# Kernel tuning notes

Measured on AMD Instinct MI355X. Metric: run time of the kernel, lower is better.

## Reference

```python
import jax, jax.numpy as jnp
import numpy as np

B, L, D, H = 4, 2048, 512, 512


def setup_inputs() -> dict:
    key = jax.random.key(0)
    ks = jax.random.split(key, 7)
    scale = D ** (-0.5)
    return {
        "x": jax.random.normal(ks[0], (B, L, D), jnp.float32),
        "hidden": jax.random.normal(ks[1], (B, D, H), jnp.float32),
        "log_base_lr": jnp.asarray(np.log(0.01), jnp.float32),
        "log_base_weight_decay": jnp.asarray(np.log(0.99), jnp.float32),
        "Wq": jax.random.normal(ks[2], (H, D), jnp.float32) * scale,
        "Wk": jax.random.normal(ks[3], (H, D), jnp.float32) * scale,
        "Wv": jax.random.normal(ks[4], (D, D), jnp.float32) * scale,
        "fc_lr_w": jax.random.normal(ks[5], (1, D), jnp.float32) * scale,
        "fc_lr_b": jnp.zeros((1,), jnp.float32),
        "fc_wd_w": jax.random.normal(ks[6], (1, D), jnp.float32) * scale,
        "fc_wd_b": jnp.zeros((1,), jnp.float32),
    }


def reference(x, hidden, log_base_lr, log_base_weight_decay, Wq, Wk, Wv,
              fc_lr_w, fc_lr_b, fc_wd_w, fc_wd_b):
    b, l, d = x.shape
    W_prev = hidden                                      # (b, d, h)
    query = jnp.einsum('bld,hd->blh', x, Wq)             # (b, l, h)
    key = jnp.einsum('bld,hd->blh', x, Wk)               # (b, l, h)
    value = jnp.einsum('bld,ed->ble', x, Wv)             # (b, l, d)

    lr = jnp.exp(log_base_lr) * jax.nn.sigmoid(
        jnp.einsum('bld,d->bl', x, fc_lr_w[0]) + fc_lr_b[0])        # (b, l)
    log_weight_decay = jnp.log(
        jnp.exp(log_base_weight_decay) * jax.nn.sigmoid(
            jnp.einsum('bld,d->bl', x, fc_wd_w[0]) + fc_wd_b[0]))   # (b, l)

    # cross-chunk decay: exp of prefix-sum of log decays
    wd_cross = jnp.exp(jnp.cumsum(log_weight_decay, axis=1))        # (b, l)

    # inner-chunk decay mask: (b, m, l), strictly-upper cumsum then upper triu
    rep = jnp.broadcast_to(log_weight_decay[:, None, :], (b, l, l))
    wd_inner = jnp.triu(jnp.exp(jnp.cumsum(jnp.triu(rep, 1), axis=2)))

    kq = jnp.einsum('blh,bmh->blm', key, query)          # (b, l, m)
    mask_kq = kq * wd_inner                              # (b, l, m)

    WpK_V = jnp.einsum('bdh,blh->bld', W_prev, key) - value         # (b, l, d)

    y_inner = -jnp.einsum('bld,bl,blm->bld', WpK_V, lr, mask_kq)
    y_cross = jnp.einsum('bdh,blh,bl->bld', W_prev, key, wd_cross)
    y = y_inner + y_cross

    W_next_inner = -jnp.einsum('bld,bl,blh->bdh', WpK_V, lr * wd_inner[:, :, -1], key)
    W_next_cross = W_prev * wd_cross[:, -1][:, None, None]
    W_next = W_next_inner + W_next_cross
    return (y, W_next)
```

## Files before the change

### kernel.cpp

```cpp
#include <hip/hip_runtime.h>
#include <cstdint>
#include <cstddef>

#define B_ 4
#define L_ 2048
#define D_ 512
#define H_ 512
#define CH 64
#define NC (L_ / CH)
#define NS 4

typedef unsigned short u16;
typedef __attribute__((ext_vector_type(8))) short short8v;
typedef __attribute__((ext_vector_type(4))) float f32x4;

typedef __attribute__((address_space(3))) unsigned lds_uint;
typedef const __attribute__((address_space(1))) unsigned glob_uint;

__device__ __forceinline__ void glds16(const u16* g, const u16* l) {
    __builtin_amdgcn_global_load_lds((glob_uint*)g, (lds_uint*)l, 16, 0, 0);
}

__device__ __forceinline__ u16 bf16_rne(float x) {
    union { float f; unsigned u; } v; v.f = x;
    unsigned r = v.u + 0x7fffu + ((v.u >> 16) & 1u);
    return (u16)(r >> 16);
}
__device__ __forceinline__ float bf16_tof(u16 h) {
    union { unsigned u; float f; } v; v.u = ((unsigned)h) << 16;
    return v.f;
}

__global__ __launch_bounds__(256) void k_prep(
    const float* __restrict__ x, const float* __restrict__ flr_w, const float* __restrict__ flr_b,
    const float* __restrict__ fwd_w, const float* __restrict__ fwd_b,
    const float* __restrict__ lblr, const float* __restrict__ lbwd,
    float* __restrict__ lr, float* __restrict__ lwd, float* __restrict__ wd,
    u16* __restrict__ xh)
{
    int bx = blockIdx.x;
    int wave = threadIdx.x >> 6;
    int lane = threadIdx.x & 63;
    int row  = bx * 4 + wave;
    const float4* xr = (const float4*)(x + (size_t)row * D_);
    const float4* wl = (const float4*)flr_w;
    const float4* ww = (const float4*)fwd_w;
    float zl = 0.f, zw = 0.f;
#pragma unroll
    for (int i = 0; i < 2; ++i) {
        int idx = lane + i * 64;
        float4 xv = xr[idx];
        float4 av = wl[idx];
        float4 bv = ww[idx];
        zl += xv.x*av.x + xv.y*av.y + xv.z*av.z + xv.w*av.w;
        zw += xv.x*bv.x + xv.y*bv.y + xv.z*bv.z + xv.w*bv.w;
        ushort4 h4;
        h4.x = bf16_rne(xv.x); h4.y = bf16_rne(xv.y);
        h4.z = bf16_rne(xv.z); h4.w = bf16_rne(xv.w);
        *(ushort4*)(xh + (size_t)row * D_ + idx * 4) = h4;
    }
#pragma unroll
    for (int off = 32; off; off >>= 1) {
        zl += __shfl_xor(zl, off, 64);
        zw += __shfl_xor(zw, off, 64);
    }
    if (lane == 0) {
        zl += flr_b[0];
        zw += fwd_b[0];
        float lrv = expf(lblr[0]) / (1.f + expf(-zl));
        float ls = (zw >= 0.f) ? (-log1pf(expf(-zw))) : (zw - log1pf(expf(zw)));
        float lw = lbwd[0] + ls;
        lr[row]  = lrv;
        lwd[row] = lw;
        wd[row]  = expf(lw);
    }
}

__global__ __launch_bounds__(256) void k_cumsum(
    const float* __restrict__ lwd, const float* __restrict__ lr,
    const float* __restrict__ Wq, const float* __restrict__ Wk, const float* __restrict__ Wv,
    const float* __restrict__ hid,
    u16* __restrict__ Wqh, u16* __restrict__ Wkh, u16* __restrict__ Wvh, u16* __restrict__ Wph,
    float* __restrict__ cum, float* __restrict__ wdc, float* __restrict__ c)
{
    int bx = blockIdx.x;
    if (bx >= B_) {
        int idx = bx - B_;
        int y = idx >> 8;
        const size_t DH = (size_t)D_ * H_;
        const float* s; u16* d;
        if      (y == 0) { s = Wq; d = Wqh; }
        else if (y == 1) { s = Wk; d = Wkh; }
        else if (y == 2) { s = Wv; d = Wvh; }
        else             { s = hid + (size_t)(y - 3) * DH; d = Wph + (size_t)(y - 3) * DH; }
        int i = ((idx & 255) * 256 + threadIdx.x) * 4;
        float4 v = *(const float4*)(s + i);
        ushort4 h4;
        h4.x = bf16_rne(v.x); h4.y = bf16_rne(v.y);
        h4.z = bf16_rne(v.z); h4.w = bf16_rne(v.w);
        *(ushort4*)(d + i) = h4;
        return;
    }
    int b = bx;
    int t = threadIdx.x;
    const float* in = lwd + (size_t)b * L_;
    float v[8];
    float s = 0.f;
#pragma unroll
    for (int j = 0; j < 8; ++j) { s += in[t*8 + j]; v[j] = s; }
    __shared__ float sd[256];
    __shared__ float totb;
    sd[t] = s;
    __syncthreads();
    for (int d = 1; d < 256; d <<= 1) {
        float xv = (t >= d) ? sd[t - d] : 0.f;
        __syncthreads();
        sd[t] += xv;
        __syncthreads();
    }
    float excl = sd[t] - s;
    if (t == 255) totb = sd[255];
    __syncthreads();
    float total = totb;
#pragma unroll
    for (int j = 0; j < 8; ++j) {
        int l = t*8 + j;
        float cv = excl + v[j];
        cum[(size_t)b*L_ + l] = cv;
        wdc[(size_t)b*L_ + l] = expf(cv);
        c[(size_t)b*L_ + l]   = lr[(size_t)b*L_ + l] * expf(total - cv);
    }
}


#define MFMA8(accv, A0v, A1v, B0v, B1v, B2v, B3v) \
    accv[0][0] = __builtin_amdgcn_mfma_f32_16x16x32_bf16(A0v, B0v, accv[0][0], 0, 0, 0); \
    accv[0][1] = __builtin_amdgcn_mfma_f32_16x16x32_bf16(A0v, B1v, accv[0][1], 0, 0, 0); \
    accv[0][2] = __builtin_amdgcn_mfma_f32_16x16x32_bf16(A0v, B2v, accv[0][2], 0, 0, 0); \
    accv[0][3] = __builtin_amdgcn_mfma_f32_16x16x32_bf16(A0v, B3v, accv[0][3], 0, 0, 0); \
    accv[1][0] = __builtin_amdgcn_mfma_f32_16x16x32_bf16(A1v, B0v, accv[1][0], 0, 0, 0); \
    accv[1][1] = __builtin_amdgcn_mfma_f32_16x16x32_bf16(A1v, B1v, accv[1][1], 0, 0, 0); \
    accv[1][2] = __builtin_amdgcn_mfma_f32_16x16x32_bf16(A1v, B2v, accv[1][2], 0, 0, 0); \
    accv[1][3] = __builtin_amdgcn_mfma_f32_16x16x32_bf16(A1v, B3v, accv[1][3], 0, 0, 0);

struct GemmGeom {
    size_t gA, gB0, gB1;
    int dA, dB0, dB1;
    int offA[2], offB[4];
};
__device__ __forceinline__ void gg_init(GemmGeom& G, int lda, int ldb, int m0, int n0) {
    const int tid  = threadIdx.x;
    const int lane = tid & 63;
    const int wv = tid >> 6, wm = wv >> 1, wn_ = wv & 1;
    const int rA = tid >> 2;
    G.gA = (size_t)(m0 + rA) * lda + (((tid & 3) ^ ((rA >> 1) & 3)) * 8);
    G.dA = wv * 1024;
    {
        int r = tid >> 2, s = tid & 3;
        G.gB0 = (size_t)(n0 + r) * ldb + ((s ^ ((r >> 1) & 3)) * 8);
        G.dB0 = wv * 1024;
        int flat = 256 + tid;
        r = flat >> 2; s = flat & 3;
        G.gB1 = (size_t)(n0 + r) * ldb + ((s ^ ((r >> 1) & 3)) * 8);
        G.dB1 = 4096 + wv * 1024;
    }
#pragma unroll
    for (int mf = 0; mf < 2; ++mf) {
        int ra = wm * 32 + mf * 16 + (lane & 15);
        G.offA[mf] = ra * 64 + (((lane >> 4) ^ ((ra >> 1) & 3)) * 16);
    }
#pragma unroll
    for (int nf = 0; nf < 4; ++nf) {
        int rb = wn_ * 64 + nf * 16 + (lane & 15);
        G.offB[nf] = rb * 64 + (((lane >> 4) ^ ((rb >> 1) & 3)) * 16);
    }
}

__device__ __forceinline__ void mfma_nt_dualB(
    char* smem, const u16* __restrict__ A_g,
    const u16* __restrict__ B0_g, const u16* __restrict__ B1_g,
    int lda, int ldb, int K, int m0, int n0, f32x4 acc0[2][4], f32x4 acc1[2][4])
{
    GemmGeom G; gg_init(G, lda, ldb, m0, n0);
    auto stage = [&](int bi, int k0) {
        glds16(A_g  + G.gA  + k0, (const u16*)(smem + bi * 4096 + G.dA));
        glds16(B0_g + G.gB0 + k0, (const u16*)(smem + 8192  + bi * 8192 + G.dB0));
        glds16(B0_g + G.gB1 + k0, (const u16*)(smem + 8192  + bi * 8192 + G.dB1));
        glds16(B1_g + G.gB0 + k0, (const u16*)(smem + 24576 + bi * 8192 + G.dB0));
        glds16(B1_g + G.gB1 + k0, (const u16*)(smem + 24576 + bi * 8192 + G.dB1));
    };
    const int nt = K >> 5;
    stage(0, 0);
    if (nt > 1) stage(1, 32);
    for (int t = 0; t < nt; ++t) {
        const int bi = t & 1;
        if (t + 1 < nt) asm volatile("s_waitcnt vmcnt(5)" ::: "memory");
        else            asm volatile("s_waitcnt vmcnt(0)" ::: "memory");
        __builtin_amdgcn_s_barrier();
        asm volatile("" ::: "memory");
        const char* bA  = smem + bi * 4096;
        const char* bB0 = smem + 8192  + bi * 8192;
        const char* bB1 = smem + 24576 + bi * 8192;
        short8v a0 = *(const short8v*)(bA + G.offA[0]);
        short8v a1 = *(const short8v*)(bA + G.offA[1]);
        short8v p0 = *(const short8v*)(bB0 + G.offB[0]);
        short8v p1 = *(const short8v*)(bB0 + G.offB[1]);
        short8v p2 = *(const short8v*)(bB0 + G.offB[2]);
        short8v p3 = *(const short8v*)(bB0 + G.offB[3]);
        short8v q0 = *(const short8v*)(bB1 + G.offB[0]);
        short8v q1 = *(const short8v*)(bB1 + G.offB[1]);
        short8v q2 = *(const short8v*)(bB1 + G.offB[2]);
        short8v q3 = *(const short8v*)(bB1 + G.offB[3]);
        __builtin_amdgcn_s_setprio(1);
        MFMA8(acc0, a0, a1, p0, p1, p2, p3)
        MFMA8(acc1, a0, a1, q0, q1, q2, q3)
        __builtin_amdgcn_s_setprio(0);
        asm volatile("" ::: "memory");
        __builtin_amdgcn_s_barrier();
        asm volatile("" ::: "memory");
        if (t + 2 < nt) stage(bi, (t + 2) << 5);
    }
}

__device__ __forceinline__ void mfma_nt_dualAB(
    char* smem, const u16* __restrict__ A0_g, const u16* __restrict__ A1_g,
    const u16* __restrict__ B0_g, const u16* __restrict__ B1_g,
    int lda, int ldb, int K, int m0, int n0, f32x4 acc0[2][4], f32x4 acc1[2][4])
{
    GemmGeom G; gg_init(G, lda, ldb, m0, n0);
    auto stage = [&](int bi, int k0) {
        glds16(A0_g + G.gA  + k0, (const u16*)(smem + bi * 4096 + G.dA));
        glds16(A1_g + G.gA  + k0, (const u16*)(smem + 8192 + bi * 4096 + G.dA));
        glds16(B0_g + G.gB0 + k0, (const u16*)(smem + 16384 + bi * 8192 + G.dB0));
        glds16(B0_g + G.gB1 + k0, (const u16*)(smem + 16384 + bi * 8192 + G.dB1));
        glds16(B1_g + G.gB0 + k0, (const u16*)(smem + 32768 + bi * 8192 + G.dB0));
        glds16(B1_g + G.gB1 + k0, (const u16*)(smem + 32768 + bi * 8192 + G.dB1));
    };
    const int nt = K >> 5;
    stage(0, 0);
    if (nt > 1) stage(1, 32);
    for (int t = 0; t < nt; ++t) {
        const int bi = t & 1;
        if (t + 1 < nt) asm volatile("s_waitcnt vmcnt(6)" ::: "memory");
        else            asm volatile("s_waitcnt vmcnt(0)" ::: "memory");
        __builtin_amdgcn_s_barrier();
        asm volatile("" ::: "memory");
        const char* bA0 = smem + bi * 4096;
        const char* bA1 = smem + 8192  + bi * 4096;
        const char* bB0 = smem + 16384 + bi * 8192;
        const char* bB1 = smem + 32768 + bi * 8192;
        short8v a0 = *(const short8v*)(bA0 + G.offA[0]);
        short8v a1 = *(const short8v*)(bA0 + G.offA[1]);
        short8v c0 = *(const short8v*)(bA1 + G.offA[0]);
        short8v c1 = *(const short8v*)(bA1 + G.offA[1]);
        short8v p0 = *(const short8v*)(bB0 + G.offB[0]);
        short8v p1 = *(const short8v*)(bB0 + G.offB[1]);
        short8v p2 = *(const short8v*)(bB0 + G.offB[2]);
        short8v p3 = *(const short8v*)(bB0 + G.offB[3]);
        short8v q0 = *(const short8v*)(bB1 + G.offB[0]);
        short8v q1 = *(const short8v*)(bB1 + G.offB[1]);
        short8v q2 = *(const short8v*)(bB1 + G.offB[2]);
        short8v q3 = *(const short8v*)(bB1 + G.offB[3]);
        __builtin_amdgcn_s_setprio(1);
        MFMA8(acc0, a0, a1, p0, p1, p2, p3)
        MFMA8(acc1, c0, c1, q0, q1, q2, q3)
        __builtin_amdgcn_s_setprio(0);
        asm volatile("" ::: "memory");
        __builtin_amdgcn_s_barrier();
        asm volatile("" ::: "memory");
        if (t + 2 < nt) stage(bi, (t + 2) << 5);
    }
}

__global__ __launch_bounds__(256) void k_mfma_qk(
    const u16* __restrict__ xh,
    const u16* __restrict__ Wqh, const u16* __restrict__ Wkh,
    const float* __restrict__ cvec, const float* __restrict__ wd,
    u16* __restrict__ kh, u16* __restrict__ kcth, u16* __restrict__ Gloc)
{
    __shared__ __align__(16) char smem[40960 + 256];
    int flat = blockIdx.x + 4 * blockIdx.y;
    flat = (flat & 7) * 64 + (flat >> 3);
    int n0 = (flat & 3) * 128;
    int m0 = (flat >> 2) * 64;
    f32x4 accq[2][4], acck[2][4];
#pragma unroll
    for (int i = 0; i < 2; ++i)
#pragma unroll
    for (int j = 0; j < 4; ++j) { accq[i][j] = 0.f; acck[i][j] = 0.f; }
    mfma_nt_dualB(smem, xh, Wqh, Wkh, D_, D_, D_, m0, n0, accq, acck);

    const int lane = threadIdx.x & 63;
    const int wv = threadIdx.x >> 6, wm = wv >> 1, wn_ = wv & 1;
    const int colq = lane & 15, rq = lane >> 4;

#pragma unroll
    for (int mf = 0; mf < 2; ++mf) {
        int grow0 = m0 + wm*32 + mf*16 + rq*4;
#pragma unroll
        for (int nf = 0; nf < 4; ++nf) {
            int gc = n0 + wn_*64 + nf*16 + colq;
            f32x4 a = acck[mf][nf];
            ushort4 hc;
#pragma unroll
            for (int r = 0; r < 4; ++r) {
                int gr = grow0 + r;
                kh[(size_t)gr * H_ + gc] = bf16_rne(a[r]);
                ((u16*)&hc)[r] = bf16_rne(cvec[gr] * a[r]);
            }
            int b = grow0 >> 11, lloc = grow0 & 2047;
            size_t tbase = (size_t)b * (H_ * L_) + (size_t)gc * L_ + lloc;
            *(ushort4*)(kcth + tbase) = hc;
        }
    }

    u16* g = (u16*)smem;
    float* p = (float*)(smem + 40960);
#pragma unroll
    for (int mf = 0; mf < 2; ++mf) {
        int rl0 = wm*32 + mf*16 + rq*4;
#pragma unroll
        for (int nf = 0; nf < 4; ++nf) {
            int cl = wn_*64 + nf*16 + colq;
#pragma unroll
            for (int r = 0; r < 4; ++r)
                g[(rl0 + r)*128 + cl] = bf16_rne(accq[mf][nf][r]);
        }
    }
    if (threadIdx.x < 64) p[threadIdx.x] = wd[m0 + threadIdx.x];
    __syncthreads();
    if (threadIdx.x < 128) {
        int col = threadIdx.x;
        float G = bf16_tof(g[63*128 + col]);
        for (int l = 62; l >= 0; --l) {
            float qv = bf16_tof(g[l*128 + col]);
            G = fmaf(p[l + 1], G, qv);
            g[l*128 + col] = bf16_rne(G);
        }
    }
    __syncthreads();
    int row = threadIdx.x >> 2, c0 = (threadIdx.x & 3) * 32;
    u16* dst = Gloc + (size_t)(m0 + row) * H_ + n0 + c0;
#pragma unroll
    for (int j = 0; j < 4; ++j)
        *(int4*)(dst + j*8) = *(const int4*)&g[row*128 + c0 + j*8];
}

__global__ __launch_bounds__(64) void k_scan_carry(
    const float* __restrict__ cum, const u16* __restrict__ Gloc, float* __restrict__ Gs)
{
    int b = blockIdx.x;
    int h = blockIdx.y * 64 + threadIdx.x;
    __shared__ float dec[NC];
    const float* cb = cum + (size_t)b * L_;
    if (threadIdx.x < NC - 1) dec[threadIdx.x] = expf(cb[(threadIdx.x + 1) * CH] - cb[threadIdx.x * CH]);
    __syncthreads();
    const u16* g = Gloc + (size_t)b * L_ * H_ + h;
    float* gs = Gs + (size_t)b * NC * H_ + h;
    float v[NC];
#pragma unroll
    for (int c = 0; c < NC; ++c)
        v[c] = bf16_tof(g[(size_t)(c * CH) * H_]);
    float G = v[NC - 1];
    gs[(size_t)(NC - 1) * H_] = G;
#pragma unroll
    for (int c = NC - 2; c >= 0; --c) {
        G = fmaf(dec[c], G, v[c]);
        gs[(size_t)c * H_] = G;
    }
}

__global__ __launch_bounds__(256) void k_sdot(
    const u16* __restrict__ kh,
    const u16* __restrict__ Gloc, const float* __restrict__ Gs,
    const float* __restrict__ cum, float* __restrict__ S)
{
    int wave = threadIdx.x >> 6, lane = threadIdx.x & 63;
    int row = blockIdx.x * 4 + wave;
    int b = row >> 11, l = row & 2047;
    int c = l / CH;
    float a = 0.f;
    const float* gsr = Gs;
    if (c < NC - 1) {
        a = expf(cum[((size_t)b << 11) + (size_t)((c + 1) * CH)] - cum[row]);
        gsr = Gs + ((size_t)(b * NC + c + 1)) * H_;
    }
    const u16* khr = kh + (size_t)row * H_;
    const u16* glr = Gloc + (size_t)row * H_;
    const float4* gq = (const float4*)gsr;
    float s = 0.f;
    int base = lane * 8;
    ushort4 h0 = *(const ushort4*)(khr + base);
    ushort4 h1 = *(const ushort4*)(khr + base + 4);
    ushort4 g0 = *(const ushort4*)(glr + base);
    ushort4 g1 = *(const ushort4*)(glr + base + 4);
    float4 s0 = gq[lane * 2];
    float4 s1 = gq[lane * 2 + 1];
    s += bf16_tof(h0.x) * fmaf(a, s0.x, bf16_tof(g0.x));
    s += bf16_tof(h0.y) * fmaf(a, s0.y, bf16_tof(g0.y));
    s += bf16_tof(h0.z) * fmaf(a, s0.z, bf16_tof(g0.z));
    s += bf16_tof(h0.w) * fmaf(a, s0.w, bf16_tof(g0.w));
    s += bf16_tof(h1.x) * fmaf(a, s1.x, bf16_tof(g1.x));
    s += bf16_tof(h1.y) * fmaf(a, s1.y, bf16_tof(g1.y));
    s += bf16_tof(h1.z) * fmaf(a, s1.z, bf16_tof(g1.z));
    s += bf16_tof(h1.w) * fmaf(a, s1.w, bf16_tof(g1.w));
#pragma unroll
    for (int off = 32; off; off >>= 1) s += __shfl_xor(s, off, 64);
    if (lane == 0) S[row] = s;
}

__global__ __launch_bounds__(256) void k_mfma_ev(
    const u16* __restrict__ kh, const u16* __restrict__ xh,
    const u16* __restrict__ Wph, const u16* __restrict__ Wvh,
    const float* __restrict__ lr, const float* __restrict__ S, const float* __restrict__ wdc,
    float* __restrict__ y, u16* __restrict__ Eth)
{
    __shared__ __align__(16) char smem[49152];
    int flat = blockIdx.x + 4 * (blockIdx.y + 32 * blockIdx.z);
    flat = (flat & 7) * 64 + (flat >> 3);
    int n0 = (flat & 3) * 128;
    int m0 = ((flat >> 2) & 31) * 64;
    int b  = flat >> 7;
    f32x4 acce[2][4], accv[2][4];
#pragma unroll
    for (int i = 0; i < 2; ++i)
#pragma unroll
    for (int j = 0; j < 4; ++j) { acce[i][j] = 0.f; accv[i][j] = 0.f; }
    mfma_nt_dualAB(smem, kh + (size_t)b * L_ * H_, xh + (size_t)b * L_ * D_,
                   Wph + (size_t)b * D_ * H_, Wvh,
                   H_, H_, H_, m0, n0, acce, accv);

    const int lane = threadIdx.x & 63;
    const int wv = threadIdx.x >> 6, wm = wv >> 1, wn_ = wv & 1;
    const int colq = lane & 15, rq = lane >> 4;
#pragma unroll
    for (int mf = 0; mf < 2; ++mf) {
        int grow0 = m0 + wm*32 + mf*16 + rq*4;
#pragma unroll
        for (int nf = 0; nf < 4; ++nf) {
            int gc = n0 + wn_*64 + nf*16 + colq;
            f32x4 ae = acce[mf][nf];
            f32x4 av = accv[mf][nf];
            ushort4 he;
#pragma unroll
            for (int r = 0; r < 4; ++r) {
                int gr = grow0 + r;
                size_t grow = (size_t)b * L_ + gr;
                size_t gi = grow * D_ + gc;
                float e = ae[r] - av[r];
                float ay = -lr[grow] * S[grow];
                y[gi] = e * ay + ae[r] * wdc[grow];
                ((u16*)&he)[r] = bf16_rne(e);
            }
            size_t tbase = (size_t)b * (D_ * L_) + (size_t)gc * L_ + grow0;
            *(ushort4*)(Eth + tbase) = he;
        }
    }
}

__device__ __forceinline__ void mfma_nt_1t(
    char* smem,
    const u16* __restrict__ A_g, const u16* __restrict__ B_g,
    int lda, int ldb, int K, int m0, int n0, f32x4 acc[2][4])
{
    GemmGeom G; gg_init(G, lda, ldb, m0, n0);
    auto stage = [&](int bi, int k0) {
        glds16(A_g + G.gA  + k0, (const u16*)(smem + bi * 4096 + G.dA));
        glds16(B_g + G.gB0 + k0, (const u16*)(smem + 8192 + bi * 8192 + G.dB0));
        glds16(B_g + G.gB1 + k0, (const u16*)(smem + 8192 + bi * 8192 + G.dB1));
    };
    const int nt = K >> 5;
    stage(0, 0);
    if (nt > 1) stage(1, 32);
    for (int t = 0; t < nt; ++t) {
        const int bi = t & 1;
        if (t + 1 < nt) asm volatile("s_waitcnt vmcnt(3)" ::: "memory");
        else            asm volatile("s_waitcnt vmcnt(0)" ::: "memory");
        __builtin_amdgcn_s_barrier();
        asm volatile("" ::: "memory");
        const char* bA = smem + bi * 4096;
        const char* bB = smem + 8192 + bi * 8192;
        short8v a0 = *(const short8v*)(bA + G.offA[0]);
        short8v a1 = *(const short8v*)(bA + G.offA[1]);
        short8v p0 = *(const short8v*)(bB + G.offB[0]);
        short8v p1 = *(const short8v*)(bB + G.offB[1]);
        short8v p2 = *(const short8v*)(bB + G.offB[2]);
        short8v p3 = *(const short8v*)(bB + G.offB[3]);
        __builtin_amdgcn_s_setprio(1);
        MFMA8(acc, a0, a1, p0, p1, p2, p3)
        __builtin_amdgcn_s_setprio(0);
        asm volatile("" ::: "memory");
        __builtin_amdgcn_s_barrier();
        asm volatile("" ::: "memory");
        if (t + 2 < nt) stage(bi, (t + 2) << 5);
    }
}

__global__ __launch_bounds__(256) void k_mfma_wn(
    const u16* __restrict__ Eth, const u16* __restrict__ kcth,
    u16* __restrict__ wp)
{
    __shared__ __align__(16) char smem[24576];
    int flat = blockIdx.x + 4 * (blockIdx.y + 8 * blockIdx.z);
    flat = (flat & 7) * 64 + (flat >> 3);
    int n0 = (flat & 3) * 128;
    int m0 = ((flat >> 2) & 7) * 64;
    int z  = flat >> 5;
    int b = z >> 2, s = z & 3;
    f32x4 acc[2][4];
#pragma unroll
    for (int i = 0; i < 2; ++i)
#pragma unroll
    for (int j = 0; j < 4; ++j) acc[i][j] = 0.f;
    const size_t pa = (size_t)b * (D_ * L_) + (size_t)s * (L_ / NS);
    const size_t pb = (size_t)b * (H_ * L_) + (size_t)s * (L_ / NS);
    mfma_nt_1t(smem, Eth + pa, kcth + pb, L_, L_, L_ / NS, m0, n0, acc);

    u16* out = wp + (size_t)z * D_ * H_;
    const int lane = threadIdx.x & 63;
    const int wv = threadIdx.x >> 6, wm = wv >> 1, wn_ = wv & 1;
    const int colq = lane & 15, rq = lane >> 4;
#pragma unroll
    for (int mf = 0; mf < 2; ++mf) {
        int grow0 = m0 + wm*32 + mf*16 + rq*4;
#pragma unroll
        for (int nf = 0; nf < 4; ++nf) {
            int gc = n0 + wn_*64 + nf*16 + colq;
            f32x4 a = acc[mf][nf];
#pragma unroll
            for (int r = 0; r < 4; ++r) out[(size_t)(grow0 + r) * H_ + gc] = bf16_rne(a[r]);
        }
    }
}

__global__ __launch_bounds__(256) void k_wnext_reduce(
    const float* __restrict__ Wp, const u16* __restrict__ wp, const float* __restrict__ wdc,
    float* __restrict__ outw)
{
    size_t g = (size_t)blockIdx.x * 256 + threadIdx.x;
    size_t per = (size_t)D_ * H_ / 4;
    int b = (int)(g / per);
    size_t r = g % per;
    float wl = wdc[(size_t)b * L_ + (L_ - 1)];
    float4 w0 = ((const float4*)Wp)[g];
    float4 o;
    o.x = wl * w0.x; o.y = wl * w0.y; o.z = wl * w0.z; o.w = wl * w0.w;
#pragma unroll
    for (int s = 0; s < NS; ++s) {
        ushort4 p = ((const ushort4*)wp)[(size_t)(b * NS + s) * per + r];
        o.x -= bf16_tof(p.x); o.y -= bf16_tof(p.y);
        o.z -= bf16_tof(p.z); o.w -= bf16_tof(p.w);
    }
    ((float4*)outw)[g] = o;
}

extern "C" void kernel_launch(void* const* d_in, const int* in_sizes, int n_in,
                              void* d_out, int out_size, void* d_ws, size_t ws_size,
                              hipStream_t stream)
{
    (void)in_sizes; (void)n_in; (void)out_size; (void)ws_size;
    const float* x    = (const float*)d_in[0];
    const float* hid  = (const float*)d_in[1];
    const float* lblr = (const float*)d_in[2];
    const float* lbwd = (const float*)d_in[3];
    const float* Wq   = (const float*)d_in[4];
    const float* Wk   = (const float*)d_in[5];
    const float* Wv   = (const float*)d_in[6];
    const float* flrw = (const float*)d_in[7];
    const float* flrb = (const float*)d_in[8];
    const float* fwdw = (const float*)d_in[9];
    const float* fwdb = (const float*)d_in[10];
    float* out = (float*)d_out;

    const size_t BL  = (size_t)B_ * L_;
    const size_t BLH = BL * H_;
    const size_t DH  = (size_t)D_ * H_;

    char* w = (char*)d_ws;
    u16* Gloc_  = (u16*)w;   w += BLH * 2;
    u16* xh_    = (u16*)w;   w += BLH * 2;
    u16* kh_    = (u16*)w;   w += BLH * 2;
    u16* kcth_  = (u16*)w;   w += BLH * 2;
    u16* Eth_   = (u16*)w;   w += BLH * 2;
    u16* Wqh_   = (u16*)w;   w += DH * 2;
    u16* Wkh_   = (u16*)w;   w += DH * 2;
    u16* Wvh_   = (u16*)w;   w += DH * 2;
    u16* Wph_   = (u16*)w;   w += (size_t)B_ * DH * 2;
    float* lr_  = (float*)w; w += BL * 4;
    float* lwd_ = (float*)w; w += BL * 4;
    float* wd_  = (float*)w; w += BL * 4;
    float* cum_ = (float*)w; w += BL * 4;
    float* wdc_ = (float*)w; w += BL * 4;
    float* c_   = (float*)w; w += BL * 4;
    float* S_   = (float*)w; w += BL * 4;
    float* Gs_  = (float*)w; w += (size_t)B_ * NC * H_ * 4;

    u16* wp_ = Gloc_;

    k_prep<<<2048, 256, 0, stream>>>(x, flrw, flrb, fwdw, fwdb, lblr, lbwd,
                                     lr_, lwd_, wd_, xh_);
    k_cumsum<<<B_ + 7 * 256, 256, 0, stream>>>(lwd_, lr_, Wq, Wk, Wv, hid,
                                               Wqh_, Wkh_, Wvh_, Wph_,
                                               cum_, wdc_, c_);
    k_mfma_qk<<<dim3(4, 128), 256, 0, stream>>>(xh_, Wqh_, Wkh_, c_, wd_,
                                                kh_, kcth_, Gloc_);
    k_scan_carry<<<dim3(B_, 8), 64, 0, stream>>>(cum_, Gloc_, Gs_);
    k_sdot<<<2048, 256, 0, stream>>>(kh_, Gloc_, Gs_, cum_, S_);
    k_mfma_ev<<<dim3(4, 32, B_), 256, 0, stream>>>(kh_, xh_, Wph_, Wvh_,
                                                   lr_, S_, wdc_, out, Eth_);
    k_mfma_wn<<<dim3(4, 8, 16), 256, 0, stream>>>(Eth_, kcth_, wp_);
    k_wnext_reduce<<<1024, 256, 0, stream>>>(hid, wp_, wdc_, out + BLH);
}
```

Measured before the change: 76.90 us.

## Enlarge MFMA GEMM tiles to 128x128 with triple-buffered LDS pipeline

The three MFMA GEMM kernels move from 64x128 to 128x128 block tiles, so each wave now computes 4x4 MFMA fragments. This doubles register-level reuse and halves the number of blocks to 256, one per CU. The LDS staging goes from double to triple buffering, which removes the trailing barrier in each k-step and issues prefetches right after the wait. The Gloc in-block decay scan is split across all 256 threads to cover the two 64-row halves. The cost is much larger LDS use (up to 96KB per block), launch_bounds limiting occupancy to one block, and higher register pressure.

```diff
diff --git a/kernel.cpp b/kernel.cpp
--- a/kernel.cpp
+++ b/kernel.cpp
@@ -133,180 +133,224 @@
 }
 
 
-#define MFMA8(accv, A0v, A1v, B0v, B1v, B2v, B3v) \
-    accv[0][0] = __builtin_amdgcn_mfma_f32_16x16x32_bf16(A0v, B0v, accv[0][0], 0, 0, 0); \
-    accv[0][1] = __builtin_amdgcn_mfma_f32_16x16x32_bf16(A0v, B1v, accv[0][1], 0, 0, 0); \
-    accv[0][2] = __builtin_amdgcn_mfma_f32_16x16x32_bf16(A0v, B2v, accv[0][2], 0, 0, 0); \
-    accv[0][3] = __builtin_amdgcn_mfma_f32_16x16x32_bf16(A0v, B3v, accv[0][3], 0, 0, 0); \
-    accv[1][0] = __builtin_amdgcn_mfma_f32_16x16x32_bf16(A1v, B0v, accv[1][0], 0, 0, 0); \
-    accv[1][1] = __builtin_amdgcn_mfma_f32_16x16x32_bf16(A1v, B1v, accv[1][1], 0, 0, 0); \
-    accv[1][2] = __builtin_amdgcn_mfma_f32_16x16x32_bf16(A1v, B2v, accv[1][2], 0, 0, 0); \
-    accv[1][3] = __builtin_amdgcn_mfma_f32_16x16x32_bf16(A1v, B3v, accv[1][3], 0, 0, 0);
-
-struct GemmGeom {
-    size_t gA, gB0, gB1;
-    int dA, dB0, dB1;
-    int offA[2], offB[4];
-};
-__device__ __forceinline__ void gg_init(GemmGeom& G, int lda, int ldb, int m0, int n0) {
-    const int tid  = threadIdx.x;
-    const int lane = tid & 63;
-    const int wv = tid >> 6, wm = wv >> 1, wn_ = wv & 1;
-    const int rA = tid >> 2;
-    G.gA = (size_t)(m0 + rA) * lda + (((tid & 3) ^ ((rA >> 1) & 3)) * 8);
-    G.dA = wv * 1024;
-    {
-        int r = tid >> 2, s = tid & 3;
-        G.gB0 = (size_t)(n0 + r) * ldb + ((s ^ ((r >> 1) & 3)) * 8);
-        G.dB0 = wv * 1024;
-        int flat = 256 + tid;
-        r = flat >> 2; s = flat & 3;
-        G.gB1 = (size_t)(n0 + r) * ldb + ((s ^ ((r >> 1) & 3)) * 8);
-        G.dB1 = 4096 + wv * 1024;
-    }
-#pragma unroll
-    for (int mf = 0; mf < 2; ++mf) {
-        int ra = wm * 32 + mf * 16 + (lane & 15);
-        G.offA[mf] = ra * 64 + (((lane >> 4) ^ ((ra >> 1) & 3)) * 16);
-    }
-#pragma unroll
-    for (int nf = 0; nf < 4; ++nf) {
-        int rb = wn_ * 64 + nf * 16 + (lane & 15);
-        G.offB[nf] = rb * 64 + (((lane >> 4) ^ ((rb >> 1) & 3)) * 16);
-    }
-}
-
-__device__ __forceinline__ void mfma_nt_dualB(
+__device__ __forceinline__ void tile_src(int base_row, int ld, size_t& g0, size_t& g1) {
+    int tid = threadIdx.x;
+    int r = tid >> 2;
+    int sw = ((tid & 3) ^ ((r >> 1) & 3)) * 8;
+    g0 = (size_t)(base_row + r) * ld + sw;
+    g1 = g0 + (size_t)64 * ld;
+}
+__device__ __forceinline__ int frag_off(int wbase, int f) {
+    int lane = threadIdx.x & 63;
+    int ra = wbase + f * 16 + (lane & 15);
+    return ra * 64 + (((lane >> 4) ^ ((ra >> 1) & 3)) * 16);
+}
+__device__ __forceinline__ void mfma44(f32x4 acc[4][4], const short8v a[4], const short8v b[4]) {
+#pragma unroll
+    for (int i = 0; i < 4; ++i)
+#pragma unroll
+        for (int j = 0; j < 4; ++j)
+            acc[i][j] = __builtin_amdgcn_mfma_f32_16x16x32_bf16(a[i], b[j], acc[i][j], 0, 0, 0);
+}
+
+__device__ __forceinline__ void core_dualB(
     char* smem, const u16* __restrict__ A_g,
     const u16* __restrict__ B0_g, const u16* __restrict__ B1_g,
-    int lda, int ldb, int K, int m0, int n0, f32x4 acc0[2][4], f32x4 acc1[2][4])
-{
-    GemmGeom G; gg_init(G, lda, ldb, m0, n0);
+    int lda, int ldb, int K, int m0, int n0, f32x4 acc0[4][4], f32x4 acc1[4][4])
+{
+    const int wv = threadIdx.x >> 6;
+    const int wm = wv >> 1, wn = wv & 1;
+    size_t aLo, aHi, bLo, bHi;
+    tile_src(m0, lda, aLo, aHi);
+    tile_src(n0, ldb, bLo, bHi);
+    const int dLo = wv * 1024, dHi = 4096 + wv * 1024;
+    int offA[4], offB[4];
+#pragma unroll
+    for (int f = 0; f < 4; ++f) { offA[f] = frag_off(wm * 64, f); offB[f] = frag_off(wn * 64, f); }
     auto stage = [&](int bi, int k0) {
-        glds16(A_g  + G.gA  + k0, (const u16*)(smem + bi * 4096 + G.dA));
-        glds16(B0_g + G.gB0 + k0, (const u16*)(smem + 8192  + bi * 8192 + G.dB0));
-        glds16(B0_g + G.gB1 + k0, (const u16*)(smem + 8192  + bi * 8192 + G.dB1));
-        glds16(B1_g + G.gB0 + k0, (const u16*)(smem + 24576 + bi * 8192 + G.dB0));
-        glds16(B1_g + G.gB1 + k0, (const u16*)(smem + 24576 + bi * 8192 + G.dB1));
+        glds16(A_g  + aLo + k0, (const u16*)(smem + bi * 8192 + dLo));
+        glds16(A_g  + aHi + k0, (const u16*)(smem + bi * 8192 + dHi));
+        glds16(B0_g + bLo + k0, (const u16*)(smem + 24576 + bi * 8192 + dLo));
+        glds16(B0_g + bHi + k0, (const u16*)(smem + 24576 + bi * 8192 + dHi));
+        glds16(B1_g + bLo + k0, (const u16*)(smem + 49152 + bi * 8192 + dLo));
+        glds16(B1_g + bHi + k0, (const u16*)(smem + 49152 + bi * 8192 + dHi));
     };
     const int nt = K >> 5;
     stage(0, 0);
-    if (nt > 1) stage(1, 32);
+    stage(1, 32);
+    int bi = 0, bs = 2;
     for (int t = 0; t < nt; ++t) {
-        const int bi = t & 1;
-        if (t + 1 < nt) asm volatile("s_waitcnt vmcnt(5)" ::: "memory");
-        else            asm volatile("s_waitcnt vmcnt(0)" ::: "memory");
-        __builtin_amdgcn_s_barrier();
-        asm volatile("" ::: "memory");
-        const char* bA  = smem + bi * 4096;
-        const char* bB0 = smem + 8192  + bi * 8192;
-        const char* bB1 = smem + 24576 + bi * 8192;
-        short8v a0 = *(const short8v*)(bA + G.offA[0]);
-        short8v a1 = *(const short8v*)(bA + G.offA[1]);
-        short8v p0 = *(const short8v*)(bB0 + G.offB[0]);
-        short8v p1 = *(const short8v*)(bB0 + G.offB[1]);
-        short8v p2 = *(const short8v*)(bB0 + G.offB[2]);
-        short8v p3 = *(const short8v*)(bB0 + G.offB[3]);
-        short8v q0 = *(const short8v*)(bB1 + G.offB[0]);
-        short8v q1 = *(const short8v*)(bB1 + G.offB[1]);
-        short8v q2 = *(const short8v*)(bB1 + G.offB[2]);
-        short8v q3 = *(const short8v*)(bB1 + G.offB[3]);
-        __builtin_amdgcn_s_setprio(1);
-        MFMA8(acc0, a0, a1, p0, p1, p2, p3)
-        MFMA8(acc1, a0, a1, q0, q1, q2, q3)
-        __builtin_amdgcn_s_setprio(0);
-        asm volatile("" ::: "memory");
-        __builtin_amdgcn_s_barrier();
-        asm volatile("" ::: "memory");
-        if (t + 2 < nt) stage(bi, (t + 2) << 5);
-    }
-}
-
-__device__ __forceinline__ void mfma_nt_dualAB(
-    char* smem, const u16* __restrict__ A0_g, const u16* __restrict__ A1_g,
-    const u16* __restrict__ B0_g, const u16* __restrict__ B1_g,
-    int lda, int ldb, int K, int m0, int n0, f32x4 acc0[2][4], f32x4 acc1[2][4])
-{
-    GemmGeom G; gg_init(G, lda, ldb, m0, n0);
-    auto stage = [&](int bi, int k0) {
-        glds16(A0_g + G.gA  + k0, (const u16*)(smem + bi * 4096 + G.dA));
-        glds16(A1_g + G.gA  + k0, (const u16*)(smem + 8192 + bi * 4096 + G.dA));
-        glds16(B0_g + G.gB0 + k0, (const u16*)(smem + 16384 + bi * 8192 + G.dB0));
-        glds16(B0_g + G.gB1 + k0, (const u16*)(smem + 16384 + bi * 8192 + G.dB1));
-        glds16(B1_g + G.gB0 + k0, (const u16*)(smem + 32768 + bi * 8192 + G.dB0));
-        glds16(B1_g + G.gB1 + k0, (const u16*)(smem + 32768 + bi * 8192 + G.dB1));
-    };
-    const int nt = K >> 5;
-    stage(0, 0);
-    if (nt > 1) stage(1, 32);
-    for (int t = 0; t < nt; ++t) {
-        const int bi = t & 1;
         if (t + 1 < nt) asm volatile("s_waitcnt vmcnt(6)" ::: "memory");
         else            asm volatile("s_waitcnt vmcnt(0)" ::: "memory");
         __builtin_amdgcn_s_barrier();
         asm volatile("" ::: "memory");
-        const char* bA0 = smem + bi * 4096;
-        const char* bA1 = smem + 8192  + bi * 4096;
-        const char* bB0 = smem + 16384 + bi * 8192;
-        const char* bB1 = smem + 32768 + bi * 8192;
-        short8v a0 = *(const short8v*)(bA0 + G.offA[0]);
-        short8v a1 = *(const short8v*)(bA0 + G.offA[1]);
-        short8v c0 = *(const short8v*)(bA1 + G.offA[0]);
-        short8v c1 = *(const short8v*)(bA1 + G.offA[1]);
-        short8v p0 = *(const short8v*)(bB0 + G.offB[0]);
-        short8v p1 = *(const short8v*)(bB0 + G.offB[1]);
-        short8v p2 = *(const short8v*)(bB0 + G.offB[2]);
-        short8v p3 = *(const short8v*)(bB0 + G.offB[3]);
-        short8v q0 = *(const short8v*)(bB1 + G.offB[0]);
-        short8v q1 = *(const short8v*)(bB1 + G.offB[1]);
-        short8v q2 = *(const short8v*)(bB1 + G.offB[2]);
-        short8v q3 = *(const short8v*)(bB1 + G.offB[3]);
+        if (t + 2 < nt) stage(bs, (t + 2) << 5);
+        const char* bA  = smem + bi * 8192;
+        const char* bB0 = smem + 24576 + bi * 8192;
+        const char* bB1 = smem + 49152 + bi * 8192;
+        short8v a[4], p[4], q[4];
+#pragma unroll
+        for (int f = 0; f < 4; ++f) {
+            a[f] = *(const short8v*)(bA  + offA[f]);
+            p[f] = *(const short8v*)(bB0 + offB[f]);
+            q[f] = *(const short8v*)(bB1 + offB[f]);
+        }
         __builtin_amdgcn_s_setprio(1);
-        MFMA8(acc0, a0, a1, p0, p1, p2, p3)
-        MFMA8(acc1, c0, c1, q0, q1, q2, q3)
+        mfma44(acc0, a, p);
+        mfma44(acc1, a, q);
         __builtin_amdgcn_s_setprio(0);
         asm volatile("" ::: "memory");
+        bi = (bi == 2) ? 0 : bi + 1;
+        bs = (bs == 2) ? 0 : bs + 1;
+    }
+    asm volatile("" ::: "memory");
+    __builtin_amdgcn_s_barrier();
+}
+
+__device__ __forceinline__ void core_dualAB(
+    char* smem, const u16* __restrict__ A0_g, const u16* __restrict__ A1_g,
+    const u16* __restrict__ B0_g, const u16* __restrict__ B1_g,
+    int lda, int ldb, int K, int m0, int n0, f32x4 acc0[4][4], f32x4 acc1[4][4])
+{
+    const int wv = threadIdx.x >> 6;
+    const int wm = wv >> 1, wn = wv & 1;
+    size_t aLo, aHi, bLo, bHi;
+    tile_src(m0, lda, aLo, aHi);
+    tile_src(n0, ldb, bLo, bHi);
+    const int dLo = wv * 1024, dHi = 4096 + wv * 1024;
+    int offA[4], offB[4];
+#pragma unroll
+    for (int f = 0; f < 4; ++f) { offA[f] = frag_off(wm * 64, f); offB[f] = frag_off(wn * 64, f); }
+    auto stage = [&](int bi, int k0) {
+        glds16(A0_g + aLo + k0, (const u16*)(smem + bi * 8192 + dLo));
+        glds16(A0_g + aHi + k0, (const u16*)(smem + bi * 8192 + dHi));
+        glds16(A1_g + aLo + k0, (const u16*)(smem + 24576 + bi * 8192 + dLo));
+        glds16(A1_g + aHi + k0, (const u16*)(smem + 24576 + bi * 8192 + dHi));
+        glds16(B0_g + bLo + k0, (const u16*)(smem + 49152 + bi * 8192 + dLo));
+        glds16(B0_g + bHi + k0, (const u16*)(smem + 49152 + bi * 8192 + dHi));
+        glds16(B1_g + bLo + k0, (const u16*)(smem + 73728 + bi * 8192 + dLo));
+        glds16(B1_g + bHi + k0, (const u16*)(smem + 73728 + bi * 8192 + dHi));
+    };
+    const int nt = K >> 5;
+    stage(0, 0);
+    stage(1, 32);
+    int bi = 0, bs = 2;
+    for (int t = 0; t < nt; ++t) {
+        if (t + 1 < nt) asm volatile("s_waitcnt vmcnt(8)" ::: "memory");
+        else            asm volatile("s_waitcnt vmcnt(0)" ::: "memory");
         __builtin_amdgcn_s_barrier();
         asm volatile("" ::: "memory");
-        if (t + 2 < nt) stage(bi, (t + 2) << 5);
-    }
-}
-
-__global__ __launch_bounds__(256) void k_mfma_qk(
+        if (t + 2 < nt) stage(bs, (t + 2) << 5);
+        const char* bA0 = smem + bi * 8192;
+        const char* bA1 = smem + 24576 + bi * 8192;
+        const char* bB0 = smem + 49152 + bi * 8192;
+        const char* bB1 = smem + 73728 + bi * 8192;
+        short8v a[4], c[4], p[4], q[4];
+#pragma unroll
+        for (int f = 0; f < 4; ++f) {
+            a[f] = *(const short8v*)(bA0 + offA[f]);
+            c[f] = *(const short8v*)(bA1 + offA[f]);
+            p[f] = *(const short8v*)(bB0 + offB[f]);
+            q[f] = *(const short8v*)(bB1 + offB[f]);
+        }
+        __builtin_amdgcn_s_setprio(1);
+        mfma44(acc0, a, p);
+        mfma44(acc1, c, q);
+        __builtin_amdgcn_s_setprio(0);
+        asm volatile("" ::: "memory");
+        bi = (bi == 2) ? 0 : bi + 1;
+        bs = (bs == 2) ? 0 : bs + 1;
+    }
+    asm volatile("" ::: "memory");
+    __builtin_amdgcn_s_barrier();
+}
+
+__device__ __forceinline__ void core_single(
+    char* smem, const u16* __restrict__ A_g, const u16* __restrict__ B_g,
+    int lda, int ldb, int K, int m0, int n0, f32x4 acc[4][4])
+{
+    const int wv = threadIdx.x >> 6;
+    const int wm = wv >> 1, wn = wv & 1;
+    size_t aLo, aHi, bLo, bHi;
+    tile_src(m0, lda, aLo, aHi);
+    tile_src(n0, ldb, bLo, bHi);
+    const int dLo = wv * 1024, dHi = 4096 + wv * 1024;
+    int offA[4], offB[4];
+#pragma unroll
+    for (int f = 0; f < 4; ++f) { offA[f] = frag_off(wm * 64, f); offB[f] = frag_off(wn * 64, f); }
+    auto stage = [&](int bi, int k0) {
+        glds16(A_g + aLo + k0, (const u16*)(smem + bi * 8192 + dLo));
+        glds16(A_g + aHi + k0, (const u16*)(smem + bi * 8192 + dHi));
+        glds16(B_g + bLo + k0, (const u16*)(smem + 24576 + bi * 8192 + dLo));
+        glds16(B_g + bHi + k0, (const u16*)(smem + 24576 + bi * 8192 + dHi));
+    };
+    const int nt = K >> 5;
+    stage(0, 0);
+    stage(1, 32);
+    int bi = 0, bs = 2;
+    for (int t = 0; t < nt; ++t) {
+        if (t + 1 < nt) asm volatile("s_waitcnt vmcnt(4)" ::: "memory");
+        else            asm volatile("s_waitcnt vmcnt(0)" ::: "memory");
+        __builtin_amdgcn_s_barrier();
+        asm volatile("" ::: "memory");
+        if (t + 2 < nt) stage(bs, (t + 2) << 5);
+        const char* bA = smem + bi * 8192;
+        const char* bB = smem + 24576 + bi * 8192;
+        short8v a[4], p[4];
+#pragma unroll
+        for (int f = 0; f < 4; ++f) {
+            a[f] = *(const short8v*)(bA + offA[f]);
+            p[f] = *(const short8v*)(bB + offB[f]);
+        }
+        __builtin_amdgcn_s_setprio(1);
+        mfma44(acc, a, p);
+        __builtin_amdgcn_s_setprio(0);
+        asm volatile("" ::: "memory");
+        bi = (bi == 2) ? 0 : bi + 1;
+        bs = (bs == 2) ? 0 : bs + 1;
+    }
+    asm volatile("" ::: "memory");
+    __builtin_amdgcn_s_barrier();
+}
+
+__global__ __launch_bounds__(256, 1) void k_mfma_qk(
     const u16* __restrict__ xh,
     const u16* __restrict__ Wqh, const u16* __restrict__ Wkh,
     const float* __restrict__ cvec, const float* __restrict__ wd,
     u16* __restrict__ kh, u16* __restrict__ kcth, u16* __restrict__ Gloc)
 {
-    __shared__ __align__(16) char smem[40960 + 256];
-    int flat = blockIdx.x + 4 * blockIdx.y;
-    flat = (flat & 7) * 64 + (flat >> 3);
+    __shared__ __align__(16) char smem[73728];
+    __shared__ float pwd[128];
+    int flat = blockIdx.x;
+    flat = (flat & 7) * 32 + (flat >> 3);
     int n0 = (flat & 3) * 128;
-    int m0 = (flat >> 2) * 64;
-    f32x4 accq[2][4], acck[2][4];
-#pragma unroll
-    for (int i = 0; i < 2; ++i)
+    int m0 = (flat >> 2) * 128;
+    f32x4 accq[4][4], acck[4][4];
+#pragma unroll
+    for (int i = 0; i < 4; ++i)
 #pragma unroll
     for (int j = 0; j < 4; ++j) { accq[i][j] = 0.f; acck[i][j] = 0.f; }
-    mfma_nt_dualB(smem, xh, Wqh, Wkh, D_, D_, D_, m0, n0, accq, acck);
+    core_dualB(smem, xh, Wqh, Wkh, D_, D_, D_, m0, n0, accq, acck);
 
     const int lane = threadIdx.x & 63;
-    const int wv = threadIdx.x >> 6, wm = wv >> 1, wn_ = wv & 1;
+    const int wv = threadIdx.x >> 6, wm = wv >> 1, wn = wv & 1;
     const int colq = lane & 15, rq = lane >> 4;
 
 #pragma unroll
-    for (int mf = 0; mf < 2; ++mf) {
-        int grow0 = m0 + wm*32 + mf*16 + rq*4;
+    for (int mf = 0; mf < 4; ++mf) {
+        int grow0 = m0 + wm*64 + mf*16 + rq*4;
+        float cv[4];
+#pragma unroll
+        for (int r = 0; r < 4; ++r) cv[r] = cvec[grow0 + r];
 #pragma unroll
         for (int nf = 0; nf < 4; ++nf) {
-            int gc = n0 + wn_*64 + nf*16 + colq;
+            int gc = n0 + wn*64 + nf*16 + colq;
             f32x4 a = acck[mf][nf];
             ushort4 hc;
 #pragma unroll
             for (int r = 0; r < 4; ++r) {
-                int gr = grow0 + r;
-                kh[(size_t)gr * H_ + gc] = bf16_rne(a[r]);
-                ((u16*)&hc)[r] = bf16_rne(cvec[gr] * a[r]);
+                kh[(size_t)(grow0 + r) * H_ + gc] = bf16_rne(a[r]);
+                ((u16*)&hc)[r] = bf16_rne(cv[r] * a[r]);
             }
             int b = grow0 >> 11, lloc = grow0 & 2047;
             size_t tbase = (size_t)b * (H_ * L_) + (size_t)gc * L_ + lloc;
@@ -315,34 +359,34 @@
     }
 
     u16* g = (u16*)smem;
-    float* p = (float*)(smem + 40960);
-#pragma unroll
-    for (int mf = 0; mf < 2; ++mf) {
-        int rl0 = wm*32 + mf*16 + rq*4;
+#pragma unroll
+    for (int mf = 0; mf < 4; ++mf) {
+        int rl0 = wm*64 + mf*16 + rq*4;
 #pragma unroll
         for (int nf = 0; nf < 4; ++nf) {
-            int cl = wn_*64 + nf*16 + colq;
+            int cl = wn*64 + nf*16 + colq;
 #pragma unroll
             for (int r = 0; r < 4; ++r)
                 g[(rl0 + r)*128 + cl] = bf16_rne(accq[mf][nf][r]);
         }
     }
-    if (threadIdx.x < 64) p[threadIdx.x] = wd[m0 + threadIdx.x];
+    if (threadIdx.x < 128) pwd[threadIdx.x] = wd[m0 + threadIdx.x];
     __syncthreads();
-    if (threadIdx.x < 128) {
-        int col = threadIdx.x;
-        float G = bf16_tof(g[63*128 + col]);
+    {
+        int col = threadIdx.x & 127;
+        int base = (threadIdx.x >> 7) * 64;
+        float G = bf16_tof(g[(base + 63)*128 + col]);
         for (int l = 62; l >= 0; --l) {
-            float qv = bf16_tof(g[l*128 + col]);
-            G = fmaf(p[l + 1], G, qv);
-            g[l*128 + col] = bf16_rne(G);
+            float qv = bf16_tof(g[(base + l)*128 + col]);
+            G = fmaf(pwd[base + l + 1], G, qv);
+            g[(base + l)*128 + col] = bf16_rne(G);
         }
     }
     __syncthreads();
-    int row = threadIdx.x >> 2, c0 = (threadIdx.x & 3) * 32;
+    int row = threadIdx.x >> 1, c0 = (threadIdx.x & 1) * 64;
     u16* dst = Gloc + (size_t)(m0 + row) * H_ + n0 + c0;
 #pragma unroll
-    for (int j = 0; j < 4; ++j)
+    for (int j = 0; j < 8; ++j)
         *(int4*)(dst + j*8) = *(const int4*)&g[row*128 + c0 + j*8];
 }
 
@@ -409,47 +453,51 @@
     if (lane == 0) S[row] = s;
 }
 
-__global__ __launch_bounds__(256) void k_mfma_ev(
+__global__ __launch_bounds__(256, 1) void k_mfma_ev(
     const u16* __restrict__ kh, const u16* __restrict__ xh,
     const u16* __restrict__ Wph, const u16* __restrict__ Wvh,
     const float* __restrict__ lr, const float* __restrict__ S, const float* __restrict__ wdc,
     float* __restrict__ y, u16* __restrict__ Eth)
 {
-    __shared__ __align__(16) char smem[49152];
-    int flat = blockIdx.x + 4 * (blockIdx.y + 32 * blockIdx.z);
-    flat = (flat & 7) * 64 + (flat >> 3);
+    __shared__ __align__(16) char smem[98304];
+    int flat = blockIdx.x;
+    flat = (flat & 7) * 32 + (flat >> 3);
     int n0 = (flat & 3) * 128;
-    int m0 = ((flat >> 2) & 31) * 64;
-    int b  = flat >> 7;
-    f32x4 acce[2][4], accv[2][4];
-#pragma unroll
-    for (int i = 0; i < 2; ++i)
+    int m0 = ((flat >> 2) & 15) * 128;
+    int b  = flat >> 6;
+    f32x4 acce[4][4], accv[4][4];
+#pragma unroll
+    for (int i = 0; i < 4; ++i)
 #pragma unroll
     for (int j = 0; j < 4; ++j) { acce[i][j] = 0.f; accv[i][j] = 0.f; }
-    mfma_nt_dualAB(smem, kh + (size_t)b * L_ * H_, xh + (size_t)b * L_ * D_,
-                   Wph + (size_t)b * D_ * H_, Wvh,
-                   H_, H_, H_, m0, n0, acce, accv);
+    core_dualAB(smem, kh + (size_t)b * L_ * H_, xh + (size_t)b * L_ * D_,
+                Wph + (size_t)b * D_ * H_, Wvh,
+                H_, H_, H_, m0, n0, acce, accv);
 
     const int lane = threadIdx.x & 63;
-    const int wv = threadIdx.x >> 6, wm = wv >> 1, wn_ = wv & 1;
+    const int wv = threadIdx.x >> 6, wm = wv >> 1, wn = wv & 1;
     const int colq = lane & 15, rq = lane >> 4;
 #pragma unroll
-    for (int mf = 0; mf < 2; ++mf) {
-        int grow0 = m0 + wm*32 + mf*16 + rq*4;
+    for (int mf = 0; mf < 4; ++mf) {
+        int grow0 = m0 + wm*64 + mf*16 + rq*4;
+        float ayv[4], wdv[4];
+#pragma unroll
+        for (int r = 0; r < 4; ++r) {
+            size_t grow = (size_t)b * L_ + grow0 + r;
+            ayv[r] = -lr[grow] * S[grow];
+            wdv[r] = wdc[grow];
+        }
 #pragma unroll
         for (int nf = 0; nf < 4; ++nf) {
-            int gc = n0 + wn_*64 + nf*16 + colq;
+            int gc = n0 + wn*64 + nf*16 + colq;
             f32x4 ae = acce[mf][nf];
             f32x4 av = accv[mf][nf];
             ushort4 he;
 #pragma unroll
             for (int r = 0; r < 4; ++r) {
-                int gr = grow0 + r;
-                size_t grow = (size_t)b * L_ + gr;
-                size_t gi = grow * D_ + gc;
+                size_t gi = ((size_t)b * L_ + grow0 + r) * D_ + gc;
                 float e = ae[r] - av[r];
-                float ay = -lr[grow] * S[grow];
-                y[gi] = e * ay + ae[r] * wdc[grow];
+                y[gi] = e * ayv[r] + ae[r] * wdv[r];
                 ((u16*)&he)[r] = bf16_rne(e);
             }
             size_t tbase = (size_t)b * (D_ * L_) + (size_t)gc * L_ + grow0;
@@ -458,74 +506,36 @@
     }
 }
 
-__device__ __forceinline__ void mfma_nt_1t(
-    char* smem,
-    const u16* __restrict__ A_g, const u16* __restrict__ B_g,
-    int lda, int ldb, int K, int m0, int n0, f32x4 acc[2][4])
-{
-    GemmGeom G; gg_init(G, lda, ldb, m0, n0);
-    auto stage = [&](int bi, int k0) {
-        glds16(A_g + G.gA  + k0, (const u16*)(smem + bi * 4096 + G.dA));
-        glds16(B_g + G.gB0 + k0, (const u16*)(smem + 8192 + bi * 8192 + G.dB0));
-        glds16(B_g + G.gB1 + k0, (const u16*)(smem + 8192 + bi * 8192 + G.dB1));
-    };
-    const int nt = K >> 5;
-    stage(0, 0);
-    if (nt > 1) stage(1, 32);
-    for (int t = 0; t < nt; ++t) {
-        const int bi = t & 1;
-        if (t + 1 < nt) asm volatile("s_waitcnt vmcnt(3)" ::: "memory");
-        else            asm volatile("s_waitcnt vmcnt(0)" ::: "memory");
-        __builtin_amdgcn_s_barrier();
-        asm volatile("" ::: "memory");
-        const char* bA = smem + bi * 4096;
-        const char* bB = smem + 8192 + bi * 8192;
-        short8v a0 = *(const short8v*)(bA + G.offA[0]);
-        short8v a1 = *(const short8v*)(bA + G.offA[1]);
-        short8v p0 = *(const short8v*)(bB + G.offB[0]);
-        short8v p1 = *(const short8v*)(bB + G.offB[1]);
-        short8v p2 = *(const short8v*)(bB + G.offB[2]);
-        short8v p3 = *(const short8v*)(bB + G.offB[3]);
-        __builtin_amdgcn_s_setprio(1);
-        MFMA8(acc, a0, a1, p0, p1, p2, p3)
-        __builtin_amdgcn_s_setprio(0);
-        asm volatile("" ::: "memory");
-        __builtin_amdgcn_s_barrier();
-        asm volatile("" ::: "memory");
-        if (t + 2 < nt) stage(bi, (t + 2) << 5);
-    }
-}
-
-__global__ __launch_bounds__(256) void k_mfma_wn(
+__global__ __launch_bounds__(256, 1) void k_mfma_wn(
     const u16* __restrict__ Eth, const u16* __restrict__ kcth,
     u16* __restrict__ wp)
 {
-    __shared__ __align__(16) char smem[24576];
-    int flat = blockIdx.x + 4 * (blockIdx.y + 8 * blockIdx.z);
-    flat = (flat & 7) * 64 + (flat >> 3);
+    __shared__ __align__(16) char smem[49152];
+    int flat = blockIdx.x;
+    flat = (flat & 7) * 32 + (flat >> 3);
     int n0 = (flat & 3) * 128;
-    int m0 = ((flat >> 2) & 7) * 64;
-    int z  = flat >> 5;
+    int m0 = ((flat >> 2) & 3) * 128;
+    int z  = flat >> 4;
     int b = z >> 2, s = z & 3;
-    f32x4 acc[2][4];
-#pragma unroll
-    for (int i = 0; i < 2; ++i)
+    f32x4 acc[4][4];
+#pragma unroll
+    for (int i = 0; i < 4; ++i)
 #pragma unroll
     for (int j = 0; j < 4; ++j) acc[i][j] = 0.f;
     const size_t pa = (size_t)b * (D_ * L_) + (size_t)s * (L_ / NS);
     const size_t pb = (size_t)b * (H_ * L_) + (size_t)s * (L_ / NS);
-    mfma_nt_1t(smem, Eth + pa, kcth + pb, L_, L_, L_ / NS, m0, n0, acc);
+    core_single(smem, Eth + pa, kcth + pb, L_, L_, L_ / NS, m0, n0, acc);
 
     u16* out = wp + (size_t)z * D_ * H_;
     const int lane = threadIdx.x & 63;
-    const int wv = threadIdx.x >> 6, wm = wv >> 1, wn_ = wv & 1;
+    const int wv = threadIdx.x >> 6, wm = wv >> 1, wn = wv & 1;
     const int colq = lane & 15, rq = lane >> 4;
 #pragma unroll
-    for (int mf = 0; mf < 2; ++mf) {
-        int grow0 = m0 + wm*32 + mf*16 + rq*4;
+    for (int mf = 0; mf < 4; ++mf) {
+        int grow0 = m0 + wm*64 + mf*16 + rq*4;
 #pragma unroll
         for (int nf = 0; nf < 4; ++nf) {
-            int gc = n0 + wn_*64 + nf*16 + colq;
+            int gc = n0 + wn*64 + nf*16 + colq;
             f32x4 a = acc[mf][nf];
 #pragma unroll
             for (int r = 0; r < 4; ++r) out[(size_t)(grow0 + r) * H_ + gc] = bf16_rne(a[r]);
@@ -602,12 +612,12 @@
     k_cumsum<<<B_ + 7 * 256, 256, 0, stream>>>(lwd_, lr_, Wq, Wk, Wv, hid,
                                                Wqh_, Wkh_, Wvh_, Wph_,
                                                cum_, wdc_, c_);
-    k_mfma_qk<<<dim3(4, 128), 256, 0, stream>>>(xh_, Wqh_, Wkh_, c_, wd_,
-                                                kh_, kcth_, Gloc_);
+    k_mfma_qk<<<256, 256, 0, stream>>>(xh_, Wqh_, Wkh_, c_, wd_,
+                                       kh_, kcth_, Gloc_);
     k_scan_carry<<<dim3(B_, 8), 64, 0, stream>>>(cum_, Gloc_, Gs_);
     k_sdot<<<2048, 256, 0, stream>>>(kh_, Gloc_, Gs_, cum_, S_);
-    k_mfma_ev<<<dim3(4, 32, B_), 256, 0, stream>>>(kh_, xh_, Wph_, Wvh_,
-                                                   lr_, S_, wdc_, out, Eth_);
-    k_mfma_wn<<<dim3(4, 8, 16), 256, 0, stream>>>(Eth_, kcth_, wp_);
+    k_mfma_ev<<<256, 256, 0, stream>>>(kh_, xh_, Wph_, Wvh_,
+                                       lr_, S_, wdc_, out, Eth_);
+    k_mfma_wn<<<256, 256, 0, stream>>>(Eth_, kcth_, wp_);
     k_wnext_reduce<<<1024, 256, 0, stream>>>(hid, wp_, wdc_, out + BLH);
 }
```

New measurement: 82.05 us. 6.7% more time.
